# Performance work log

Hardware: AMD Instinct MI355X
Metric: run time of the kernel (lower is better)

## Reference

```python
import jax, jax.numpy as jnp
import numpy as np

E = 32      # particle_embed_dim = q/k/v head out dim
G = 2       # nof_net_types (conv groups)
NEG_SLOPE = 0.01


def _glin(x, w, b, groups):
    """Grouped 1x1 conv on (M, C, 1, 1) == grouped linear.
    x: (M, Cin), w: (Cout, Cin//groups), b: (Cout,)."""
    M = x.shape[0]
    Cout = w.shape[0]
    xg = x.reshape(M, groups, -1)                 # (M, G, Cin/G)
    wg = w.reshape(groups, Cout // groups, -1)    # (G, Cout/G, Cin/G)
    y = jnp.einsum('mgi,goi->mgo', xg, wg).reshape(M, Cout)
    return y + b


def setup_inputs() -> dict:
    key = jax.random.key(0)
    ks = jax.random.split(key, 9)
    B, N = 32, 1024
    s = 0.05
    return {
        'x_e':   jax.random.normal(ks[0], (B, N, G * E), dtype=jnp.float32),
        'w_qkv': jax.random.normal(ks[1], (3 * G * E, E), dtype=jnp.float32) * s,
        'b_qkv': jax.random.normal(ks[2], (3 * G * E,), dtype=jnp.float32) * s,
        'w_h1':  jax.random.normal(ks[3], (G * E, 2 * E), dtype=jnp.float32) * s,
        'b_h1':  jax.random.normal(ks[4], (G * E,), dtype=jnp.float32) * s,
        'w_h10': jax.random.normal(ks[5], (G * E, E), dtype=jnp.float32) * s,
        'b_h10': jax.random.normal(ks[6], (G * E,), dtype=jnp.float32) * s,
        'w_h11': jax.random.normal(ks[7], (G * E, E), dtype=jnp.float32) * s,
        'b_h11': jax.random.normal(ks[8], (G * E,), dtype=jnp.float32) * s,
    }


def reference(x_e, w_qkv, b_qkv, w_h1, b_h1, w_h10, b_h10, w_h11, b_h11):
    B, N, D = x_e.shape                      # D = G*E = 64
    act = lambda z: jnp.where(z >= 0, z, NEG_SLOPE * z)

    # grouped 1x1-conv QKV projection
    qkv = _glin(x_e.reshape(B * N, D), w_qkv, b_qkv, G)        # (B*N, 3*G*E)
    qkv = qkv.reshape(B, N, G, 3, E).transpose(0, 2, 3, 1, 4)  # (B, G, 3, N, E)
    q, k, v = qkv[:, :, 0], qkv[:, :, 1], qkv[:, :, 2]         # each (B, G, N, E)

    # NOTE: module divides k by sqrt(E) and logits by sqrt(E) again -> 1/E total
    scale = 1.0 / E
    ip = jnp.einsum('bgne,bgme->bgnm', q, k) * scale           # (B, G, N, N)
    sip = jax.nn.softmax(ip, axis=-1)
    attn = jnp.einsum('bgnm,bgme->bgne', sip, v)               # (B, G, N, E)

    # concat pre-attention v with attention output, regroup per-particle
    x_xe = jnp.concatenate([v, attn], axis=3)                  # (B, G, N, 2E)
    x_xe = x_xe.transpose(0, 2, 1, 3).reshape(B * N, G * 2 * E)  # (B*N, 128)

    h = act(_glin(x_xe, w_h1, b_h1, G))
    h = act(_glin(h, w_h10, b_h10, G))
    h = act(_glin(h, w_h11, b_h11, G))
    return h.reshape(B * N, G * E, 1, 1)
```

## Files before the change

### kernel.cpp

```cpp
#include <hip/hip_runtime.h>

#define B_ 32
#define N_ 1024
#define NEG 0.01f
#define QSC (1.4426950408889634f/32.0f)

using half8  = __attribute__((ext_vector_type(8))) _Float16;
using half4  = __attribute__((ext_vector_type(4))) _Float16;
using half2  = __attribute__((ext_vector_type(2))) _Float16;
using fp16x2 = __attribute__((ext_vector_type(2))) __fp16;
using floatx4 = __attribute__((ext_vector_type(4))) float;

#if defined(__has_builtin)
#if __has_builtin(__builtin_amdgcn_exp2f)
#define EXP2(x) __builtin_amdgcn_exp2f(x)
#endif
#endif
#ifndef EXP2
#define EXP2(x) exp2f(x)
#endif

__device__ inline half2 pkcvt(float a, float b) {
    fp16x2 r = __builtin_amdgcn_cvt_pkrtz(a, b);
    return __builtin_bit_cast(half2, r);
}

__device__ inline half8 cvt8(float4 a, float4 b) {
    half2 p0 = pkcvt(a.x, a.y);
    half2 p1 = pkcvt(a.z, a.w);
    half2 p2 = pkcvt(b.x, b.y);
    half2 p3 = pkcvt(b.z, b.w);
    half8 h = { p0[0],p0[1], p1[0],p1[1], p2[0],p2[1], p3[0],p3[1] };
    return h;
}

struct __align__(16) Smem {
    _Float16 wsh[96*36];
    float    bsh[96];
    _Float16 Kst[2][128*40];
    _Float16 Vtst[2][32*136];
    union {
        _Float16 qs[128*40];
        _Float16 xs[128*72];
    } u;
    float linv[128];
    float bl1[32], bl10[32], bl11[32];
};

__global__ __launch_bounds__(256, 2) void fused_kernel(
    const float* __restrict__ x, const float* __restrict__ w_qkv, const float* __restrict__ b_qkv,
    const float* __restrict__ w_h1,  const float* __restrict__ b_h1,
    const float* __restrict__ w_h10, const float* __restrict__ b_h10,
    const float* __restrict__ w_h11, const float* __restrict__ b_h11,
    float* __restrict__ out)
{
    __shared__ Smem sm;
    int t = threadIdx.x;
    int bg = blockIdx.x >> 3;
    int qtile = blockIdx.x & 7;
    int b = bg >> 1, g = bg & 1;
    int qbase = qtile * 128;
    int lane = t & 63, w = t >> 6;
    int L15 = lane & 15, quad = lane >> 4;

    for (int idx = t; idx < 96*32; idx += 256) {
        int r = idx >> 5, c = idx & 31;
        float wv = w_qkv[(g*96 + r)*32 + c];
        sm.wsh[r*36 + c] = (_Float16)(r < 32 ? wv*QSC : wv);
    }
    if (t < 96) sm.bsh[t] = b_qkv[g*96 + t];
    if (t < 32) {
        sm.bl1[t]  = b_h1[g*32+t];
        sm.bl10[t] = b_h10[g*32+t];
        sm.bl11[t] = b_h11[g*32+t];
    }
    __syncthreads();

    half8 bwq[2], bwk[2], bwv[2];
    floatx4 cq[2], ck[2], cv[2];
    #pragma unroll
    for (int et = 0; et < 2; et++) {
        bwq[et] = *(const half8*)&sm.wsh[(     et*16 + L15)*36 + quad*8];
        bwk[et] = *(const half8*)&sm.wsh[(32 + et*16 + L15)*36 + quad*8];
        bwv[et] = *(const half8*)&sm.wsh[(64 + et*16 + L15)*36 + quad*8];
        float bq = sm.bsh[     et*16 + L15] * QSC;
        float bk = sm.bsh[32 + et*16 + L15];
        float bv = sm.bsh[64 + et*16 + L15];
        cq[et] = (floatx4){bq,bq,bq,bq};
        ck[et] = (floatx4){bk,bk,bk,bk};
        cv[et] = (floatx4){bv,bv,bv,bv};
    }

    {
        floatx4 dq[2][2];
        #pragma unroll
        for (int mt = 0; mt < 2; mt++) {
            const float* p = x + ((size_t)b*N_ + qbase + w*32 + mt*16 + L15)*64 + g*32 + quad*8;
            half8 axq = cvt8(*(const float4*)p, *(const float4*)(p + 4));
            dq[mt][0] = __builtin_amdgcn_mfma_f32_16x16x32_f16(axq, bwq[0], cq[0], 0,0,0);
            dq[mt][1] = __builtin_amdgcn_mfma_f32_16x16x32_f16(axq, bwq[1], cq[1], 0,0,0);
        }
        #pragma unroll
        for (int mt = 0; mt < 2; mt++)
            #pragma unroll
            for (int et = 0; et < 2; et++)
                #pragma unroll
                for (int r = 0; r < 4; r++)
                    sm.u.qs[(w*32 + mt*16 + quad*4 + r)*40 + et*16 + L15] =
                        (_Float16)dq[mt][et][r];
    }
    __syncthreads();
    half8 bq0 = *(const half8*)&sm.u.qs[(w*32 +      L15)*40 + quad*8];
    half8 bq1 = *(const half8*)&sm.u.qs[(w*32 + 16 + L15)*40 + quad*8];

    float4 xf0[2], xf1[2];
    auto prefetch = [&](int tile) {
        #pragma unroll
        for (int mt = 0; mt < 2; mt++) {
            const float* p = x + ((size_t)b*N_ + tile*128 + w*32 + mt*16 + L15)*64 + g*32 + quad*8;
            xf0[mt] = *(const float4*)p;
            xf1[mt] = *(const float4*)(p + 4);
        }
    };
    auto proj_tile = [&](int tile, int buf) {
        floatx4 dK[2][2], dV[2][2];
        #pragma unroll
        for (int mt = 0; mt < 2; mt++) {
            half8 axk = cvt8(xf0[mt], xf1[mt]);
            dK[mt][0] = __builtin_amdgcn_mfma_f32_16x16x32_f16(axk, bwk[0], ck[0], 0,0,0);
            dK[mt][1] = __builtin_amdgcn_mfma_f32_16x16x32_f16(axk, bwk[1], ck[1], 0,0,0);
            dV[mt][0] = __builtin_amdgcn_mfma_f32_16x16x32_f16(axk, bwv[0], cv[0], 0,0,0);
            dV[mt][1] = __builtin_amdgcn_mfma_f32_16x16x32_f16(axk, bwv[1], cv[1], 0,0,0);
        }
        #pragma unroll
        for (int mt = 0; mt < 2; mt++) {
            int rb = w*32 + mt*16 + quad*4;
            #pragma unroll
            for (int et = 0; et < 2; et++) {
                half2 k01 = pkcvt(dK[mt][et][0], dK[mt][et][1]);
                half2 k23 = pkcvt(dK[mt][et][2], dK[mt][et][3]);
                half2 v01 = pkcvt(dV[mt][et][0], dV[mt][et][1]);
                half2 v23 = pkcvt(dV[mt][et][2], dV[mt][et][3]);
                half4 vh = { v01[0], v01[1], v23[0], v23[1] };
                sm.Kst[buf][(rb+0)*40 + et*16 + L15] = k01[0];
                sm.Kst[buf][(rb+1)*40 + et*16 + L15] = k01[1];
                sm.Kst[buf][(rb+2)*40 + et*16 + L15] = k23[0];
                sm.Kst[buf][(rb+3)*40 + et*16 + L15] = k23[1];
                *(half4*)&sm.Vtst[buf][(et*16 + L15)*136 + rb] = vh;
                if (tile == qtile) {
                    #pragma unroll
                    for (int r = 0; r < 4; r++)
                        sm.u.xs[(rb + r)*72 + et*16 + L15] = vh[r];
                }
            }
        }
    };

    prefetch(0);
    proj_tile(0, 0);
    __syncthreads();

    floatx4 o00 = {0.f,0.f,0.f,0.f}, o01 = o00, o10 = o00, o11 = o00;
    float lsum0 = 0.f, lsum1 = 0.f;

    for (int kt = 0; kt < 8; kt++) {
        int cur = kt & 1;
        if (kt < 7) prefetch(kt + 1);
        #pragma unroll
        for (int mt8 = 0; mt8 < 8; mt8++) {
            half8 ak = *(const half8*)&sm.Kst[cur][(mt8*16 + L15)*40 + quad*8];
            floatx4 zz = {0.f,0.f,0.f,0.f};
            floatx4 s0 = __builtin_amdgcn_mfma_f32_16x16x32_f16(ak, bq0, zz, 0,0,0);
            floatx4 s1 = __builtin_amdgcn_mfma_f32_16x16x32_f16(ak, bq1, zz, 0,0,0);
            float p00 = EXP2(s0.x), p01 = EXP2(s0.y), p02 = EXP2(s0.z), p03 = EXP2(s0.w);
            float p10 = EXP2(s1.x), p11 = EXP2(s1.y), p12 = EXP2(s1.z), p13 = EXP2(s1.w);
            lsum0 += (p00+p01)+(p02+p03);
            lsum1 += (p10+p11)+(p12+p13);
            half2 pa = pkcvt(p00, p01);
            half2 pb = pkcvt(p02, p03);
            half2 pc = pkcvt(p10, p11);
            half2 pd = pkcvt(p12, p13);
            half4 a0 = { pa[0], pa[1], pb[0], pb[1] };
            half4 a1 = { pc[0], pc[1], pd[0], pd[1] };
            half4 bv0 = *(const half4*)&sm.Vtst[cur][      L15*136 + mt8*16 + quad*4];
            half4 bv1 = *(const half4*)&sm.Vtst[cur][(16 + L15)*136 + mt8*16 + quad*4];
            o00 = __builtin_amdgcn_mfma_f32_16x16x16f16(a0, bv0, o00, 0,0,0);
            o01 = __builtin_amdgcn_mfma_f32_16x16x16f16(a0, bv1, o01, 0,0,0);
            o10 = __builtin_amdgcn_mfma_f32_16x16x16f16(a1, bv0, o10, 0,0,0);
            o11 = __builtin_amdgcn_mfma_f32_16x16x16f16(a1, bv1, o11, 0,0,0);
        }
        if (kt < 7) proj_tile(kt + 1, 1 - cur);
        __syncthreads();
    }

    lsum0 += __shfl_xor(lsum0, 16, 64); lsum0 += __shfl_xor(lsum0, 32, 64);
    lsum1 += __shfl_xor(lsum1, 16, 64); lsum1 += __shfl_xor(lsum1, 32, 64);
    if (quad == 0) {
        sm.linv[w*32 +      L15] = 1.0f / lsum0;
        sm.linv[w*32 + 16 + L15] = 1.0f / lsum1;
    }
    __syncthreads();

    {
        const floatx4* ofr[2][2] = { {&o00,&o01}, {&o10,&o11} };
        #pragma unroll
        for (int nt = 0; nt < 2; nt++) {
            float4 li = *(const float4*)&sm.linv[w*32 + nt*16 + quad*4];
            #pragma unroll
            for (int et = 0; et < 2; et++) {
                floatx4 ov = *ofr[nt][et];
                sm.u.xs[(w*32+nt*16+quad*4+0)*72 + 32 + et*16 + L15] = (_Float16)(ov[0]*li.x);
                sm.u.xs[(w*32+nt*16+quad*4+1)*72 + 32 + et*16 + L15] = (_Float16)(ov[1]*li.y);
                sm.u.xs[(w*32+nt*16+quad*4+2)*72 + 32 + et*16 + L15] = (_Float16)(ov[2]*li.z);
                sm.u.xs[(w*32+nt*16+quad*4+3)*72 + 32 + et*16 + L15] = (_Float16)(ov[3]*li.w);
            }
        }
    }
    __syncthreads();

    half4 a1f[2][4], a2f[2][2], a3f[2][2];
    #pragma unroll
    for (int mt = 0; mt < 2; mt++) {
        #pragma unroll
        for (int kt = 0; kt < 4; kt++) {
            float4 f = *(const float4*)(w_h1 + (size_t)(g*32+mt*16+L15)*64 + kt*16 + quad*4);
            half2 ha = pkcvt(f.x, f.y);
            half2 hb = pkcvt(f.z, f.w);
            half4 h = { ha[0], ha[1], hb[0], hb[1] };
            a1f[mt][kt] = h;
        }
        #pragma unroll
        for (int kt = 0; kt < 2; kt++) {
            float4 f = *(const float4*)(w_h10 + (size_t)(g*32+mt*16+L15)*32 + kt*16 + quad*4);
            half2 ha = pkcvt(f.x, f.y);
            half2 hb = pkcvt(f.z, f.w);
            half4 h = { ha[0], ha[1], hb[0], hb[1] };
            a2f[mt][kt] = h;
            float4 f2 = *(const float4*)(w_h11 + (size_t)(g*32+mt*16+L15)*32 + kt*16 + quad*4);
            half2 hc = pkcvt(f2.x, f2.y);
            half2 hd = pkcvt(f2.z, f2.w);
            half4 h2 = { hc[0], hc[1], hd[0], hd[1] };
            a3f[mt][kt] = h2;
        }
    }

    floatx4 d1[2][2];
    #pragma unroll
    for (int mt = 0; mt < 2; mt++) {
        float4 bb = *(const float4*)&sm.bl1[mt*16 + quad*4];
        floatx4 seed = { bb.x, bb.y, bb.z, bb.w };
        d1[mt][0] = seed; d1[mt][1] = seed;
    }
    #pragma unroll
    for (int nt = 0; nt < 2; nt++)
        #pragma unroll
        for (int kt = 0; kt < 4; kt++) {
            half4 b1 = *(const half4*)&sm.u.xs[(w*32+nt*16+L15)*72 + kt*16 + quad*4];
            d1[0][nt] = __builtin_amdgcn_mfma_f32_16x16x16f16(a1f[0][kt], b1, d1[0][nt], 0,0,0);
            d1[1][nt] = __builtin_amdgcn_mfma_f32_16x16x16f16(a1f[1][kt], b1, d1[1][nt], 0,0,0);
        }
    half4 h1b[2][2];
    #pragma unroll
    for (int mt = 0; mt < 2; mt++)
        #pragma unroll
        for (int nt = 0; nt < 2; nt++) {
            float v0 = d1[mt][nt][0]; v0 = (v0>=0.f)?v0:NEG*v0;
            float v1 = d1[mt][nt][1]; v1 = (v1>=0.f)?v1:NEG*v1;
            float v2 = d1[mt][nt][2]; v2 = (v2>=0.f)?v2:NEG*v2;
            float v3 = d1[mt][nt][3]; v3 = (v3>=0.f)?v3:NEG*v3;
            half2 ha = pkcvt(v0, v1);
            half2 hb = pkcvt(v2, v3);
            half4 h = { ha[0], ha[1], hb[0], hb[1] };
            h1b[mt][nt] = h;
        }
    floatx4 d2[2][2];
    #pragma unroll
    for (int mt = 0; mt < 2; mt++) {
        float4 bb = *(const float4*)&sm.bl10[mt*16 + quad*4];
        floatx4 seed = { bb.x, bb.y, bb.z, bb.w };
        d2[mt][0] = seed; d2[mt][1] = seed;
    }
    #pragma unroll
    for (int mt = 0; mt < 2; mt++)
        #pragma unroll
        for (int nt = 0; nt < 2; nt++)
            #pragma unroll
            for (int kt = 0; kt < 2; kt++)
                d2[mt][nt] = __builtin_amdgcn_mfma_f32_16x16x16f16(a2f[mt][kt], h1b[kt][nt], d2[mt][nt], 0,0,0);
    half4 h2b[2][2];
    #pragma unroll
    for (int mt = 0; mt < 2; mt++)
        #pragma unroll
        for (int nt = 0; nt < 2; nt++) {
            float v0 = d2[mt][nt][0]; v0 = (v0>=0.f)?v0:NEG*v0;
            float v1 = d2[mt][nt][1]; v1 = (v1>=0.f)?v1:NEG*v1;
            float v2 = d2[mt][nt][2]; v2 = (v2>=0.f)?v2:NEG*v2;
            float v3 = d2[mt][nt][3]; v3 = (v3>=0.f)?v3:NEG*v3;
            half2 ha = pkcvt(v0, v1);
            half2 hb = pkcvt(v2, v3);
            half4 h = { ha[0], ha[1], hb[0], hb[1] };
            h2b[mt][nt] = h;
        }
    floatx4 d3[2][2];
    #pragma unroll
    for (int mt = 0; mt < 2; mt++) {
        float4 bb = *(const float4*)&sm.bl11[mt*16 + quad*4];
        floatx4 seed = { bb.x, bb.y, bb.z, bb.w };
        d3[mt][0] = seed; d3[mt][1] = seed;
    }
    #pragma unroll
    for (int mt = 0; mt < 2; mt++)
        #pragma unroll
        for (int nt = 0; nt < 2; nt++)
            #pragma unroll
            for (int kt = 0; kt < 2; kt++)
                d3[mt][nt] = __builtin_amdgcn_mfma_f32_16x16x16f16(a3f[mt][kt], h2b[kt][nt], d3[mt][nt], 0,0,0);
    #pragma unroll
    for (int mt = 0; mt < 2; mt++)
        #pragma unroll
        for (int nt = 0; nt < 2; nt++) {
            float4 ov;
            ov.x = d3[mt][nt][0]; ov.x = (ov.x>=0.f)?ov.x:NEG*ov.x;
            ov.y = d3[mt][nt][1]; ov.y = (ov.y>=0.f)?ov.y:NEG*ov.y;
            ov.z = d3[mt][nt][2]; ov.z = (ov.z>=0.f)?ov.z:NEG*ov.z;
            ov.w = d3[mt][nt][3]; ov.w = (ov.w>=0.f)?ov.w:NEG*ov.w;
            *(float4*)(out + ((size_t)b*N_ + qbase + w*32 + nt*16 + L15)*64 + g*32 + mt*16 + quad*4) = ov;
        }
}

extern "C" void kernel_launch(void* const* d_in, const int* in_sizes, int n_in,
                              void* d_out, int out_size, void* d_ws, size_t ws_size,
                              hipStream_t stream) {
    const float* x_e   = (const float*)d_in[0];
    const float* w_qkv = (const float*)d_in[1];
    const float* b_qkv = (const float*)d_in[2];
    const float* w_h1  = (const float*)d_in[3];
    const float* b_h1  = (const float*)d_in[4];
    const float* w_h10 = (const float*)d_in[5];
    const float* b_h10 = (const float*)d_in[6];
    const float* w_h11 = (const float*)d_in[7];
    const float* b_h11 = (const float*)d_in[8];
    float* out = (float*)d_out;

    hipLaunchKernelGGL(fused_kernel, dim3(B_*2*8), dim3(256), 0, stream,
                       x_e, w_qkv, b_qkv, w_h1, b_h1, w_h10, b_h10, w_h11, b_h11, out);
}
```

Measured before the change: 98.57 us.

## Halve query tile to 64 rows and raise occupancy with overlapped LDS

Each block now handles 64 query rows instead of 128, and streams keys in 64-row tiles over 16 iterations. The grid doubles to 1024 blocks and launch bounds allow 4 blocks per CU. Shared memory is shrunk by overlaying the weight staging, Q staging, K/V double buffers and the MLP input buffer in unions. The block's own V rows are recomputed from x after the loop instead of copied during projection. The aim is more resident waves to hide latency, at the cost of duplicating the K/V projection across twice as many blocks, twice as many barriers, and fewer MFMAs per LDS load.

```diff
diff --git a/kernel.cpp b/kernel.cpp
--- a/kernel.cpp
+++ b/kernel.cpp
@@ -35,19 +35,22 @@
 }
 
 struct __align__(16) Smem {
-    _Float16 wsh[96*36];
-    float    bsh[96];
-    _Float16 Kst[2][128*40];
-    _Float16 Vtst[2][32*136];
     union {
-        _Float16 qs[128*40];
-        _Float16 xs[128*72];
+        struct {
+            _Float16 Kst[2][64*40];
+            _Float16 Vtst[2][32*72];
+            union {
+                struct { _Float16 wsh[96*36]; float bsh[96]; } wg;
+                _Float16 qs[64*40];
+            } pq;
+        } lp;
+        _Float16 xs[64*72];
     } u;
-    float linv[128];
+    float linv[64];
     float bl1[32], bl10[32], bl11[32];
 };
 
-__global__ __launch_bounds__(256, 2) void fused_kernel(
+__global__ __launch_bounds__(256, 4) void fused_kernel(
     const float* __restrict__ x, const float* __restrict__ w_qkv, const float* __restrict__ b_qkv,
     const float* __restrict__ w_h1,  const float* __restrict__ b_h1,
     const float* __restrict__ w_h10, const float* __restrict__ b_h10,
@@ -56,19 +59,19 @@
 {
     __shared__ Smem sm;
     int t = threadIdx.x;
-    int bg = blockIdx.x >> 3;
-    int qtile = blockIdx.x & 7;
+    int bg = blockIdx.x >> 4;
+    int qtile = blockIdx.x & 15;
     int b = bg >> 1, g = bg & 1;
-    int qbase = qtile * 128;
+    int qbase = qtile * 64;
     int lane = t & 63, w = t >> 6;
     int L15 = lane & 15, quad = lane >> 4;
 
     for (int idx = t; idx < 96*32; idx += 256) {
         int r = idx >> 5, c = idx & 31;
         float wv = w_qkv[(g*96 + r)*32 + c];
-        sm.wsh[r*36 + c] = (_Float16)(r < 32 ? wv*QSC : wv);
-    }
-    if (t < 96) sm.bsh[t] = b_qkv[g*96 + t];
+        sm.u.lp.pq.wg.wsh[r*36 + c] = (_Float16)(r < 32 ? wv*QSC : wv);
+    }
+    if (t < 96) sm.u.lp.pq.wg.bsh[t] = b_qkv[g*96 + t];
     if (t < 32) {
         sm.bl1[t]  = b_h1[g*32+t];
         sm.bl10[t] = b_h10[g*32+t];
@@ -80,143 +83,116 @@
     floatx4 cq[2], ck[2], cv[2];
     #pragma unroll
     for (int et = 0; et < 2; et++) {
-        bwq[et] = *(const half8*)&sm.wsh[(     et*16 + L15)*36 + quad*8];
-        bwk[et] = *(const half8*)&sm.wsh[(32 + et*16 + L15)*36 + quad*8];
-        bwv[et] = *(const half8*)&sm.wsh[(64 + et*16 + L15)*36 + quad*8];
-        float bq = sm.bsh[     et*16 + L15] * QSC;
-        float bk = sm.bsh[32 + et*16 + L15];
-        float bv = sm.bsh[64 + et*16 + L15];
+        bwq[et] = *(const half8*)&sm.u.lp.pq.wg.wsh[(     et*16 + L15)*36 + quad*8];
+        bwk[et] = *(const half8*)&sm.u.lp.pq.wg.wsh[(32 + et*16 + L15)*36 + quad*8];
+        bwv[et] = *(const half8*)&sm.u.lp.pq.wg.wsh[(64 + et*16 + L15)*36 + quad*8];
+        float bq = sm.u.lp.pq.wg.bsh[     et*16 + L15] * QSC;
+        float bk = sm.u.lp.pq.wg.bsh[32 + et*16 + L15];
+        float bv = sm.u.lp.pq.wg.bsh[64 + et*16 + L15];
         cq[et] = (floatx4){bq,bq,bq,bq};
         ck[et] = (floatx4){bk,bk,bk,bk};
         cv[et] = (floatx4){bv,bv,bv,bv};
     }
+    __syncthreads();
 
     {
-        floatx4 dq[2][2];
-        #pragma unroll
-        for (int mt = 0; mt < 2; mt++) {
-            const float* p = x + ((size_t)b*N_ + qbase + w*32 + mt*16 + L15)*64 + g*32 + quad*8;
-            half8 axq = cvt8(*(const float4*)p, *(const float4*)(p + 4));
-            dq[mt][0] = __builtin_amdgcn_mfma_f32_16x16x32_f16(axq, bwq[0], cq[0], 0,0,0);
-            dq[mt][1] = __builtin_amdgcn_mfma_f32_16x16x32_f16(axq, bwq[1], cq[1], 0,0,0);
-        }
-        #pragma unroll
-        for (int mt = 0; mt < 2; mt++)
-            #pragma unroll
-            for (int et = 0; et < 2; et++)
-                #pragma unroll
-                for (int r = 0; r < 4; r++)
-                    sm.u.qs[(w*32 + mt*16 + quad*4 + r)*40 + et*16 + L15] =
-                        (_Float16)dq[mt][et][r];
-    }
+        const float* p = x + ((size_t)b*N_ + qbase + w*16 + L15)*64 + g*32 + quad*8;
+        half8 axq = cvt8(*(const float4*)p, *(const float4*)(p + 4));
+        floatx4 dq0 = __builtin_amdgcn_mfma_f32_16x16x32_f16(axq, bwq[0], cq[0], 0,0,0);
+        floatx4 dq1 = __builtin_amdgcn_mfma_f32_16x16x32_f16(axq, bwq[1], cq[1], 0,0,0);
+        #pragma unroll
+        for (int r = 0; r < 4; r++) {
+            sm.u.lp.pq.qs[(w*16 + quad*4 + r)*40 +      L15] = (_Float16)dq0[r];
+            sm.u.lp.pq.qs[(w*16 + quad*4 + r)*40 + 16 + L15] = (_Float16)dq1[r];
+        }
+    }
+    half8 bq = *(const half8*)&sm.u.lp.pq.qs[(w*16 + L15)*40 + quad*8];
+
+    float4 xf0, xf1;
+    auto prefetch = [&](int tile) {
+        const float* p = x + ((size_t)b*N_ + tile*64 + w*16 + L15)*64 + g*32 + quad*8;
+        xf0 = *(const float4*)p;
+        xf1 = *(const float4*)(p + 4);
+    };
+    auto proj_tile = [&](int buf) {
+        half8 axk = cvt8(xf0, xf1);
+        floatx4 dK[2], dV[2];
+        #pragma unroll
+        for (int et = 0; et < 2; et++) {
+            dK[et] = __builtin_amdgcn_mfma_f32_16x16x32_f16(axk, bwk[et], ck[et], 0,0,0);
+            dV[et] = __builtin_amdgcn_mfma_f32_16x16x32_f16(axk, bwv[et], cv[et], 0,0,0);
+        }
+        int rb = w*16 + quad*4;
+        #pragma unroll
+        for (int et = 0; et < 2; et++) {
+            half2 k01 = pkcvt(dK[et][0], dK[et][1]);
+            half2 k23 = pkcvt(dK[et][2], dK[et][3]);
+            half2 v01 = pkcvt(dV[et][0], dV[et][1]);
+            half2 v23 = pkcvt(dV[et][2], dV[et][3]);
+            half4 vh = { v01[0], v01[1], v23[0], v23[1] };
+            sm.u.lp.Kst[buf][(rb+0)*40 + et*16 + L15] = k01[0];
+            sm.u.lp.Kst[buf][(rb+1)*40 + et*16 + L15] = k01[1];
+            sm.u.lp.Kst[buf][(rb+2)*40 + et*16 + L15] = k23[0];
+            sm.u.lp.Kst[buf][(rb+3)*40 + et*16 + L15] = k23[1];
+            *(half4*)&sm.u.lp.Vtst[buf][(et*16 + L15)*72 + rb] = vh;
+        }
+    };
+
+    prefetch(0);
+    proj_tile(0);
     __syncthreads();
-    half8 bq0 = *(const half8*)&sm.u.qs[(w*32 +      L15)*40 + quad*8];
-    half8 bq1 = *(const half8*)&sm.u.qs[(w*32 + 16 + L15)*40 + quad*8];
-
-    float4 xf0[2], xf1[2];
-    auto prefetch = [&](int tile) {
-        #pragma unroll
-        for (int mt = 0; mt < 2; mt++) {
-            const float* p = x + ((size_t)b*N_ + tile*128 + w*32 + mt*16 + L15)*64 + g*32 + quad*8;
-            xf0[mt] = *(const float4*)p;
-            xf1[mt] = *(const float4*)(p + 4);
-        }
-    };
-    auto proj_tile = [&](int tile, int buf) {
-        floatx4 dK[2][2], dV[2][2];
-        #pragma unroll
-        for (int mt = 0; mt < 2; mt++) {
-            half8 axk = cvt8(xf0[mt], xf1[mt]);
-            dK[mt][0] = __builtin_amdgcn_mfma_f32_16x16x32_f16(axk, bwk[0], ck[0], 0,0,0);
-            dK[mt][1] = __builtin_amdgcn_mfma_f32_16x16x32_f16(axk, bwk[1], ck[1], 0,0,0);
-            dV[mt][0] = __builtin_amdgcn_mfma_f32_16x16x32_f16(axk, bwv[0], cv[0], 0,0,0);
-            dV[mt][1] = __builtin_amdgcn_mfma_f32_16x16x32_f16(axk, bwv[1], cv[1], 0,0,0);
-        }
-        #pragma unroll
-        for (int mt = 0; mt < 2; mt++) {
-            int rb = w*32 + mt*16 + quad*4;
-            #pragma unroll
-            for (int et = 0; et < 2; et++) {
-                half2 k01 = pkcvt(dK[mt][et][0], dK[mt][et][1]);
-                half2 k23 = pkcvt(dK[mt][et][2], dK[mt][et][3]);
-                half2 v01 = pkcvt(dV[mt][et][0], dV[mt][et][1]);
-                half2 v23 = pkcvt(dV[mt][et][2], dV[mt][et][3]);
-                half4 vh = { v01[0], v01[1], v23[0], v23[1] };
-                sm.Kst[buf][(rb+0)*40 + et*16 + L15] = k01[0];
-                sm.Kst[buf][(rb+1)*40 + et*16 + L15] = k01[1];
-                sm.Kst[buf][(rb+2)*40 + et*16 + L15] = k23[0];
-                sm.Kst[buf][(rb+3)*40 + et*16 + L15] = k23[1];
-                *(half4*)&sm.Vtst[buf][(et*16 + L15)*136 + rb] = vh;
-                if (tile == qtile) {
-                    #pragma unroll
-                    for (int r = 0; r < 4; r++)
-                        sm.u.xs[(rb + r)*72 + et*16 + L15] = vh[r];
-                }
-            }
-        }
-    };
-
-    prefetch(0);
-    proj_tile(0, 0);
-    __syncthreads();
-
-    floatx4 o00 = {0.f,0.f,0.f,0.f}, o01 = o00, o10 = o00, o11 = o00;
-    float lsum0 = 0.f, lsum1 = 0.f;
-
-    for (int kt = 0; kt < 8; kt++) {
+
+    floatx4 o0 = {0.f,0.f,0.f,0.f}, o1 = o0;
+    float lsum = 0.f;
+
+    for (int kt = 0; kt < 16; kt++) {
         int cur = kt & 1;
-        if (kt < 7) prefetch(kt + 1);
-        #pragma unroll
-        for (int mt8 = 0; mt8 < 8; mt8++) {
-            half8 ak = *(const half8*)&sm.Kst[cur][(mt8*16 + L15)*40 + quad*8];
+        if (kt < 15) prefetch(kt + 1);
+        #pragma unroll
+        for (int mt8 = 0; mt8 < 4; mt8++) {
+            half8 ak = *(const half8*)&sm.u.lp.Kst[cur][(mt8*16 + L15)*40 + quad*8];
             floatx4 zz = {0.f,0.f,0.f,0.f};
-            floatx4 s0 = __builtin_amdgcn_mfma_f32_16x16x32_f16(ak, bq0, zz, 0,0,0);
-            floatx4 s1 = __builtin_amdgcn_mfma_f32_16x16x32_f16(ak, bq1, zz, 0,0,0);
-            float p00 = EXP2(s0.x), p01 = EXP2(s0.y), p02 = EXP2(s0.z), p03 = EXP2(s0.w);
-            float p10 = EXP2(s1.x), p11 = EXP2(s1.y), p12 = EXP2(s1.z), p13 = EXP2(s1.w);
-            lsum0 += (p00+p01)+(p02+p03);
-            lsum1 += (p10+p11)+(p12+p13);
-            half2 pa = pkcvt(p00, p01);
-            half2 pb = pkcvt(p02, p03);
-            half2 pc = pkcvt(p10, p11);
-            half2 pd = pkcvt(p12, p13);
+            floatx4 s = __builtin_amdgcn_mfma_f32_16x16x32_f16(ak, bq, zz, 0,0,0);
+            float p0 = EXP2(s.x), p1 = EXP2(s.y), p2 = EXP2(s.z), p3 = EXP2(s.w);
+            lsum += (p0+p1)+(p2+p3);
+            half2 pa = pkcvt(p0, p1);
+            half2 pb = pkcvt(p2, p3);
             half4 a0 = { pa[0], pa[1], pb[0], pb[1] };
-            half4 a1 = { pc[0], pc[1], pd[0], pd[1] };
-            half4 bv0 = *(const half4*)&sm.Vtst[cur][      L15*136 + mt8*16 + quad*4];
-            half4 bv1 = *(const half4*)&sm.Vtst[cur][(16 + L15)*136 + mt8*16 + quad*4];
-            o00 = __builtin_amdgcn_mfma_f32_16x16x16f16(a0, bv0, o00, 0,0,0);
-            o01 = __builtin_amdgcn_mfma_f32_16x16x16f16(a0, bv1, o01, 0,0,0);
-            o10 = __builtin_amdgcn_mfma_f32_16x16x16f16(a1, bv0, o10, 0,0,0);
-            o11 = __builtin_amdgcn_mfma_f32_16x16x16f16(a1, bv1, o11, 0,0,0);
-        }
-        if (kt < 7) proj_tile(kt + 1, 1 - cur);
+            half4 bv0 = *(const half4*)&sm.u.lp.Vtst[cur][      L15*72 + mt8*16 + quad*4];
+            half4 bv1 = *(const half4*)&sm.u.lp.Vtst[cur][(16 + L15)*72 + mt8*16 + quad*4];
+            o0 = __builtin_amdgcn_mfma_f32_16x16x16f16(a0, bv0, o0, 0,0,0);
+            o1 = __builtin_amdgcn_mfma_f32_16x16x16f16(a0, bv1, o1, 0,0,0);
+        }
+        if (kt < 15) proj_tile(1 - cur);
         __syncthreads();
     }
 
-    lsum0 += __shfl_xor(lsum0, 16, 64); lsum0 += __shfl_xor(lsum0, 32, 64);
-    lsum1 += __shfl_xor(lsum1, 16, 64); lsum1 += __shfl_xor(lsum1, 32, 64);
-    if (quad == 0) {
-        sm.linv[w*32 +      L15] = 1.0f / lsum0;
-        sm.linv[w*32 + 16 + L15] = 1.0f / lsum1;
-    }
-    __syncthreads();
+    lsum += __shfl_xor(lsum, 16, 64); lsum += __shfl_xor(lsum, 32, 64);
+    if (quad == 0) sm.linv[w*16 + L15] = 1.0f / lsum;
 
     {
-        const floatx4* ofr[2][2] = { {&o00,&o01}, {&o10,&o11} };
-        #pragma unroll
-        for (int nt = 0; nt < 2; nt++) {
-            float4 li = *(const float4*)&sm.linv[w*32 + nt*16 + quad*4];
-            #pragma unroll
-            for (int et = 0; et < 2; et++) {
-                floatx4 ov = *ofr[nt][et];
-                sm.u.xs[(w*32+nt*16+quad*4+0)*72 + 32 + et*16 + L15] = (_Float16)(ov[0]*li.x);
-                sm.u.xs[(w*32+nt*16+quad*4+1)*72 + 32 + et*16 + L15] = (_Float16)(ov[1]*li.y);
-                sm.u.xs[(w*32+nt*16+quad*4+2)*72 + 32 + et*16 + L15] = (_Float16)(ov[2]*li.z);
-                sm.u.xs[(w*32+nt*16+quad*4+3)*72 + 32 + et*16 + L15] = (_Float16)(ov[3]*li.w);
-            }
-        }
-    }
-    __syncthreads();
+        const float* p = x + ((size_t)b*N_ + qbase + w*16 + L15)*64 + g*32 + quad*8;
+        half8 axv = cvt8(*(const float4*)p, *(const float4*)(p + 4));
+        floatx4 dv0 = __builtin_amdgcn_mfma_f32_16x16x32_f16(axv, bwv[0], cv[0], 0,0,0);
+        floatx4 dv1 = __builtin_amdgcn_mfma_f32_16x16x32_f16(axv, bwv[1], cv[1], 0,0,0);
+        #pragma unroll
+        for (int r = 0; r < 4; r++) {
+            sm.u.xs[(w*16 + quad*4 + r)*72 +      L15] = (_Float16)dv0[r];
+            sm.u.xs[(w*16 + quad*4 + r)*72 + 16 + L15] = (_Float16)dv1[r];
+        }
+    }
+    {
+        float4 li = *(const float4*)&sm.linv[w*16 + quad*4];
+        const floatx4* ofr[2] = { &o0, &o1 };
+        #pragma unroll
+        for (int et = 0; et < 2; et++) {
+            floatx4 ov = *ofr[et];
+            sm.u.xs[(w*16+quad*4+0)*72 + 32 + et*16 + L15] = (_Float16)(ov[0]*li.x);
+            sm.u.xs[(w*16+quad*4+1)*72 + 32 + et*16 + L15] = (_Float16)(ov[1]*li.y);
+            sm.u.xs[(w*16+quad*4+2)*72 + 32 + et*16 + L15] = (_Float16)(ov[2]*li.z);
+            sm.u.xs[(w*16+quad*4+3)*72 + 32 + et*16 + L15] = (_Float16)(ov[3]*li.w);
+        }
+    }
 
     half4 a1f[2][4], a2f[2][2], a3f[2][2];
     #pragma unroll
@@ -244,88 +220,73 @@
         }
     }
 
-    floatx4 d1[2][2];
+    floatx4 d1[2];
     #pragma unroll
     for (int mt = 0; mt < 2; mt++) {
         float4 bb = *(const float4*)&sm.bl1[mt*16 + quad*4];
-        floatx4 seed = { bb.x, bb.y, bb.z, bb.w };
-        d1[mt][0] = seed; d1[mt][1] = seed;
-    }
-    #pragma unroll
-    for (int nt = 0; nt < 2; nt++)
-        #pragma unroll
-        for (int kt = 0; kt < 4; kt++) {
-            half4 b1 = *(const half4*)&sm.u.xs[(w*32+nt*16+L15)*72 + kt*16 + quad*4];
-            d1[0][nt] = __builtin_amdgcn_mfma_f32_16x16x16f16(a1f[0][kt], b1, d1[0][nt], 0,0,0);
-            d1[1][nt] = __builtin_amdgcn_mfma_f32_16x16x16f16(a1f[1][kt], b1, d1[1][nt], 0,0,0);
-        }
-    half4 h1b[2][2];
+        d1[mt] = (floatx4){ bb.x, bb.y, bb.z, bb.w };
+    }
+    #pragma unroll
+    for (int kt = 0; kt < 4; kt++) {
+        half4 b1 = *(const half4*)&sm.u.xs[(w*16+L15)*72 + kt*16 + quad*4];
+        d1[0] = __builtin_amdgcn_mfma_f32_16x16x16f16(a1f[0][kt], b1, d1[0], 0,0,0);
+        d1[1] = __builtin_amdgcn_mfma_f32_16x16x16f16(a1f[1][kt], b1, d1[1], 0,0,0);
+    }
+    half4 h1b[2];
+    #pragma unroll
+    for (int mt = 0; mt < 2; mt++) {
+        float v0 = d1[mt][0]; v0 = (v0>=0.f)?v0:NEG*v0;
+        float v1 = d1[mt][1]; v1 = (v1>=0.f)?v1:NEG*v1;
+        float v2 = d1[mt][2]; v2 = (v2>=0.f)?v2:NEG*v2;
+        float v3 = d1[mt][3]; v3 = (v3>=0.f)?v3:NEG*v3;
+        half2 ha = pkcvt(v0, v1);
+        half2 hb = pkcvt(v2, v3);
+        half4 h = { ha[0], ha[1], hb[0], hb[1] };
+        h1b[mt] = h;
+    }
+    floatx4 d2[2];
+    #pragma unroll
+    for (int mt = 0; mt < 2; mt++) {
+        float4 bb = *(const float4*)&sm.bl10[mt*16 + quad*4];
+        d2[mt] = (floatx4){ bb.x, bb.y, bb.z, bb.w };
+    }
     #pragma unroll
     for (int mt = 0; mt < 2; mt++)
         #pragma unroll
-        for (int nt = 0; nt < 2; nt++) {
-            float v0 = d1[mt][nt][0]; v0 = (v0>=0.f)?v0:NEG*v0;
-            float v1 = d1[mt][nt][1]; v1 = (v1>=0.f)?v1:NEG*v1;
-            float v2 = d1[mt][nt][2]; v2 = (v2>=0.f)?v2:NEG*v2;
-            float v3 = d1[mt][nt][3]; v3 = (v3>=0.f)?v3:NEG*v3;
-            half2 ha = pkcvt(v0, v1);
-            half2 hb = pkcvt(v2, v3);
-            half4 h = { ha[0], ha[1], hb[0], hb[1] };
-            h1b[mt][nt] = h;
-        }
-    floatx4 d2[2][2];
-    #pragma unroll
-    for (int mt = 0; mt < 2; mt++) {
-        float4 bb = *(const float4*)&sm.bl10[mt*16 + quad*4];
-        floatx4 seed = { bb.x, bb.y, bb.z, bb.w };
-        d2[mt][0] = seed; d2[mt][1] = seed;
+        for (int kt = 0; kt < 2; kt++)
+            d2[mt] = __builtin_amdgcn_mfma_f32_16x16x16f16(a2f[mt][kt], h1b[kt], d2[mt], 0,0,0);
+    half4 h2b[2];
+    #pragma unroll
+    for (int mt = 0; mt < 2; mt++) {
+        float v0 = d2[mt][0]; v0 = (v0>=0.f)?v0:NEG*v0;
+        float v1 = d2[mt][1]; v1 = (v1>=0.f)?v1:NEG*v1;
+        float v2 = d2[mt][2]; v2 = (v2>=0.f)?v2:NEG*v2;
+        float v3 = d2[mt][3]; v3 = (v3>=0.f)?v3:NEG*v3;
+        half2 ha = pkcvt(v0, v1);
+        half2 hb = pkcvt(v2, v3);
+        half4 h = { ha[0], ha[1], hb[0], hb[1] };
+        h2b[mt] = h;
+    }
+    floatx4 d3[2];
+    #pragma unroll
+    for (int mt = 0; mt < 2; mt++) {
+        float4 bb = *(const float4*)&sm.bl11[mt*16 + quad*4];
+        d3[mt] = (floatx4){ bb.x, bb.y, bb.z, bb.w };
     }
     #pragma unroll
     for (int mt = 0; mt < 2; mt++)
         #pragma unroll
-        for (int nt = 0; nt < 2; nt++)
-            #pragma unroll
-            for (int kt = 0; kt < 2; kt++)
-                d2[mt][nt] = __builtin_amdgcn_mfma_f32_16x16x16f16(a2f[mt][kt], h1b[kt][nt], d2[mt][nt], 0,0,0);
-    half4 h2b[2][2];
-    #pragma unroll
-    for (int mt = 0; mt < 2; mt++)
-        #pragma unroll
-        for (int nt = 0; nt < 2; nt++) {
-            float v0 = d2[mt][nt][0]; v0 = (v0>=0.f)?v0:NEG*v0;
-            float v1 = d2[mt][nt][1]; v1 = (v1>=0.f)?v1:NEG*v1;
-            float v2 = d2[mt][nt][2]; v2 = (v2>=0.f)?v2:NEG*v2;
-            float v3 = d2[mt][nt][3]; v3 = (v3>=0.f)?v3:NEG*v3;
-            half2 ha = pkcvt(v0, v1);
-            half2 hb = pkcvt(v2, v3);
-            half4 h = { ha[0], ha[1], hb[0], hb[1] };
-            h2b[mt][nt] = h;
-        }
-    floatx4 d3[2][2];
-    #pragma unroll
-    for (int mt = 0; mt < 2; mt++) {
-        float4 bb = *(const float4*)&sm.bl11[mt*16 + quad*4];
-        floatx4 seed = { bb.x, bb.y, bb.z, bb.w };
-        d3[mt][0] = seed; d3[mt][1] = seed;
-    }
-    #pragma unroll
-    for (int mt = 0; mt < 2; mt++)
-        #pragma unroll
-        for (int nt = 0; nt < 2; nt++)
-            #pragma unroll
-            for (int kt = 0; kt < 2; kt++)
-                d3[mt][nt] = __builtin_amdgcn_mfma_f32_16x16x16f16(a3f[mt][kt], h2b[kt][nt], d3[mt][nt], 0,0,0);
-    #pragma unroll
-    for (int mt = 0; mt < 2; mt++)
-        #pragma unroll
-        for (int nt = 0; nt < 2; nt++) {
-            float4 ov;
-            ov.x = d3[mt][nt][0]; ov.x = (ov.x>=0.f)?ov.x:NEG*ov.x;
-            ov.y = d3[mt][nt][1]; ov.y = (ov.y>=0.f)?ov.y:NEG*ov.y;
-            ov.z = d3[mt][nt][2]; ov.z = (ov.z>=0.f)?ov.z:NEG*ov.z;
-            ov.w = d3[mt][nt][3]; ov.w = (ov.w>=0.f)?ov.w:NEG*ov.w;
-            *(float4*)(out + ((size_t)b*N_ + qbase + w*32 + nt*16 + L15)*64 + g*32 + mt*16 + quad*4) = ov;
-        }
+        for (int kt = 0; kt < 2; kt++)
+            d3[mt] = __builtin_amdgcn_mfma_f32_16x16x16f16(a3f[mt][kt], h2b[kt], d3[mt], 0,0,0);
+    #pragma unroll
+    for (int mt = 0; mt < 2; mt++) {
+        float4 ov;
+        ov.x = d3[mt][0]; ov.x = (ov.x>=0.f)?ov.x:NEG*ov.x;
+        ov.y = d3[mt][1]; ov.y = (ov.y>=0.f)?ov.y:NEG*ov.y;
+        ov.z = d3[mt][2]; ov.z = (ov.z>=0.f)?ov.z:NEG*ov.z;
+        ov.w = d3[mt][3]; ov.w = (ov.w>=0.f)?ov.w:NEG*ov.w;
+        *(float4*)(out + ((size_t)b*N_ + qbase + w*16 + L15)*64 + g*32 + mt*16 + quad*4) = ov;
+    }
 }
 
 extern "C" void kernel_launch(void* const* d_in, const int* in_sizes, int n_in,
@@ -342,6 +303,6 @@
     const float* b_h11 = (const float*)d_in[8];
     float* out = (float*)d_out;
 
-    hipLaunchKernelGGL(fused_kernel, dim3(B_*2*8), dim3(256), 0, stream,
+    hipLaunchKernelGGL(fused_kernel, dim3(B_*2*16), dim3(256), 0, stream,
                        x_e, w_qkv, b_qkv, w_h1, b_h1, w_h10, b_h10, w_h11, b_h11, out);
 }
```

Result: slower. 107.9 us (+9.5%).

## Deepen x prefetch, drop wave-local barriers, shrink LDS, and reorder block mapping

Applied to the files above, without the earlier changes.

The global loads of x are now double-buffered in registers and issued two tiles ahead, so load latency overlaps with more attention work. Several __syncthreads are removed where each wave only reads LDS rows it wrote itself. The QKV weight staging now shares a union with the Q/X buffers, and the V transpose stride is reduced from 136 to 132, which cuts LDS use and changes the bank mapping. The block index is remapped so all (batch, group) pairs for one query tile run together. The pre-attention V for the block's own tile is recomputed from x at the end instead of being stored conditionally inside the projection loop. In exchange, register pressure rises and there is a small amount of redundant MFMA work and global reads.

```diff
diff --git a/kernel.cpp b/kernel.cpp
--- a/kernel.cpp
+++ b/kernel.cpp
@@ -35,11 +35,10 @@
 }
 
 struct __align__(16) Smem {
-    _Float16 wsh[96*36];
-    float    bsh[96];
     _Float16 Kst[2][128*40];
-    _Float16 Vtst[2][32*136];
+    _Float16 Vtst[2][32*132];
     union {
+        struct { _Float16 wsh[96*36]; float bsh[96]; } wg;
         _Float16 qs[128*40];
         _Float16 xs[128*72];
     } u;
@@ -56,8 +55,8 @@
 {
     __shared__ Smem sm;
     int t = threadIdx.x;
-    int bg = blockIdx.x >> 3;
-    int qtile = blockIdx.x & 7;
+    int bg = blockIdx.x & 63;
+    int qtile = blockIdx.x >> 6;
     int b = bg >> 1, g = bg & 1;
     int qbase = qtile * 128;
     int lane = t & 63, w = t >> 6;
@@ -66,9 +65,9 @@
     for (int idx = t; idx < 96*32; idx += 256) {
         int r = idx >> 5, c = idx & 31;
         float wv = w_qkv[(g*96 + r)*32 + c];
-        sm.wsh[r*36 + c] = (_Float16)(r < 32 ? wv*QSC : wv);
-    }
-    if (t < 96) sm.bsh[t] = b_qkv[g*96 + t];
+        sm.u.wg.wsh[r*36 + c] = (_Float16)(r < 32 ? wv*QSC : wv);
+    }
+    if (t < 96) sm.u.wg.bsh[t] = b_qkv[g*96 + t];
     if (t < 32) {
         sm.bl1[t]  = b_h1[g*32+t];
         sm.bl10[t] = b_h10[g*32+t];
@@ -80,84 +79,75 @@
     floatx4 cq[2], ck[2], cv[2];
     #pragma unroll
     for (int et = 0; et < 2; et++) {
-        bwq[et] = *(const half8*)&sm.wsh[(     et*16 + L15)*36 + quad*8];
-        bwk[et] = *(const half8*)&sm.wsh[(32 + et*16 + L15)*36 + quad*8];
-        bwv[et] = *(const half8*)&sm.wsh[(64 + et*16 + L15)*36 + quad*8];
-        float bq = sm.bsh[     et*16 + L15] * QSC;
-        float bk = sm.bsh[32 + et*16 + L15];
-        float bv = sm.bsh[64 + et*16 + L15];
+        bwq[et] = *(const half8*)&sm.u.wg.wsh[(     et*16 + L15)*36 + quad*8];
+        bwk[et] = *(const half8*)&sm.u.wg.wsh[(32 + et*16 + L15)*36 + quad*8];
+        bwv[et] = *(const half8*)&sm.u.wg.wsh[(64 + et*16 + L15)*36 + quad*8];
+        float bq = sm.u.wg.bsh[     et*16 + L15] * QSC;
+        float bk = sm.u.wg.bsh[32 + et*16 + L15];
+        float bv = sm.u.wg.bsh[64 + et*16 + L15];
         cq[et] = (floatx4){bq,bq,bq,bq};
         ck[et] = (floatx4){bk,bk,bk,bk};
         cv[et] = (floatx4){bv,bv,bv,bv};
     }
+    __syncthreads();
 
     {
-        floatx4 dq[2][2];
         #pragma unroll
         for (int mt = 0; mt < 2; mt++) {
             const float* p = x + ((size_t)b*N_ + qbase + w*32 + mt*16 + L15)*64 + g*32 + quad*8;
             half8 axq = cvt8(*(const float4*)p, *(const float4*)(p + 4));
-            dq[mt][0] = __builtin_amdgcn_mfma_f32_16x16x32_f16(axq, bwq[0], cq[0], 0,0,0);
-            dq[mt][1] = __builtin_amdgcn_mfma_f32_16x16x32_f16(axq, bwq[1], cq[1], 0,0,0);
-        }
-        #pragma unroll
-        for (int mt = 0; mt < 2; mt++)
-            #pragma unroll
-            for (int et = 0; et < 2; et++)
-                #pragma unroll
-                for (int r = 0; r < 4; r++)
-                    sm.u.qs[(w*32 + mt*16 + quad*4 + r)*40 + et*16 + L15] =
-                        (_Float16)dq[mt][et][r];
-    }
-    __syncthreads();
+            floatx4 dq0 = __builtin_amdgcn_mfma_f32_16x16x32_f16(axq, bwq[0], cq[0], 0,0,0);
+            floatx4 dq1 = __builtin_amdgcn_mfma_f32_16x16x32_f16(axq, bwq[1], cq[1], 0,0,0);
+            #pragma unroll
+            for (int r = 0; r < 4; r++) {
+                sm.u.qs[(w*32 + mt*16 + quad*4 + r)*40 +      L15] = (_Float16)dq0[r];
+                sm.u.qs[(w*32 + mt*16 + quad*4 + r)*40 + 16 + L15] = (_Float16)dq1[r];
+            }
+        }
+    }
     half8 bq0 = *(const half8*)&sm.u.qs[(w*32 +      L15)*40 + quad*8];
     half8 bq1 = *(const half8*)&sm.u.qs[(w*32 + 16 + L15)*40 + quad*8];
 
-    float4 xf0[2], xf1[2];
-    auto prefetch = [&](int tile) {
+    float4 xf0[2][2], xf1[2][2];
+    auto prefetch = [&](int tile, int pp) {
         #pragma unroll
         for (int mt = 0; mt < 2; mt++) {
             const float* p = x + ((size_t)b*N_ + tile*128 + w*32 + mt*16 + L15)*64 + g*32 + quad*8;
-            xf0[mt] = *(const float4*)p;
-            xf1[mt] = *(const float4*)(p + 4);
+            xf0[pp][mt] = *(const float4*)p;
+            xf1[pp][mt] = *(const float4*)(p + 4);
         }
     };
-    auto proj_tile = [&](int tile, int buf) {
-        floatx4 dK[2][2], dV[2][2];
+    auto proj_tile = [&](int buf, int pp) {
         #pragma unroll
         for (int mt = 0; mt < 2; mt++) {
-            half8 axk = cvt8(xf0[mt], xf1[mt]);
-            dK[mt][0] = __builtin_amdgcn_mfma_f32_16x16x32_f16(axk, bwk[0], ck[0], 0,0,0);
-            dK[mt][1] = __builtin_amdgcn_mfma_f32_16x16x32_f16(axk, bwk[1], ck[1], 0,0,0);
-            dV[mt][0] = __builtin_amdgcn_mfma_f32_16x16x32_f16(axk, bwv[0], cv[0], 0,0,0);
-            dV[mt][1] = __builtin_amdgcn_mfma_f32_16x16x32_f16(axk, bwv[1], cv[1], 0,0,0);
-        }
-        #pragma unroll
-        for (int mt = 0; mt < 2; mt++) {
+            half8 axk = cvt8(xf0[pp][mt], xf1[pp][mt]);
+            floatx4 dK[2], dV[2];
+            #pragma unroll
+            for (int et = 0; et < 2; et++) {
+                dK[et] = __builtin_amdgcn_mfma_f32_16x16x32_f16(axk, bwk[et], ck[et], 0,0,0);
+                dV[et] = __builtin_amdgcn_mfma_f32_16x16x32_f16(axk, bwv[et], cv[et], 0,0,0);
+            }
             int rb = w*32 + mt*16 + quad*4;
             #pragma unroll
             for (int et = 0; et < 2; et++) {
-                half2 k01 = pkcvt(dK[mt][et][0], dK[mt][et][1]);
-                half2 k23 = pkcvt(dK[mt][et][2], dK[mt][et][3]);
-                half2 v01 = pkcvt(dV[mt][et][0], dV[mt][et][1]);
-                half2 v23 = pkcvt(dV[mt][et][2], dV[mt][et][3]);
+                half2 k01 = pkcvt(dK[et][0], dK[et][1]);
+                half2 k23 = pkcvt(dK[et][2], dK[et][3]);
+                half2 v01 = pkcvt(dV[et][0], dV[et][1]);
+                half2 v23 = pkcvt(dV[et][2], dV[et][3]);
                 half4 vh = { v01[0], v01[1], v23[0], v23[1] };
                 sm.Kst[buf][(rb+0)*40 + et*16 + L15] = k01[0];
                 sm.Kst[buf][(rb+1)*40 + et*16 + L15] = k01[1];
                 sm.Kst[buf][(rb+2)*40 + et*16 + L15] = k23[0];
                 sm.Kst[buf][(rb+3)*40 + et*16 + L15] = k23[1];
-                *(half4*)&sm.Vtst[buf][(et*16 + L15)*136 + rb] = vh;
-                if (tile == qtile) {
-                    #pragma unroll
-                    for (int r = 0; r < 4; r++)
-                        sm.u.xs[(rb + r)*72 + et*16 + L15] = vh[r];
-                }
+                *(half4*)&sm.Vtst[buf][(et*16 + L15)*132 + rb] = vh;
             }
         }
     };
 
-    prefetch(0);
+    prefetch(0, 0);
     proj_tile(0, 0);
+    prefetch(1, 1);
+    prefetch(2, 0);
     __syncthreads();
 
     floatx4 o00 = {0.f,0.f,0.f,0.f}, o01 = o00, o10 = o00, o11 = o00;
@@ -165,10 +155,9 @@
 
     for (int kt = 0; kt < 8; kt++) {
         int cur = kt & 1;
-        if (kt < 7) prefetch(kt + 1);
-        #pragma unroll
-        for (int mt8 = 0; mt8 < 8; mt8++) {
-            half8 ak = *(const half8*)&sm.Kst[cur][(mt8*16 + L15)*40 + quad*8];
+        #pragma unroll
+        for (int m8 = 0; m8 < 8; m8++) {
+            half8 ak = *(const half8*)&sm.Kst[cur][(m8*16 + L15)*40 + quad*8];
             floatx4 zz = {0.f,0.f,0.f,0.f};
             floatx4 s0 = __builtin_amdgcn_mfma_f32_16x16x32_f16(ak, bq0, zz, 0,0,0);
             floatx4 s1 = __builtin_amdgcn_mfma_f32_16x16x32_f16(ak, bq1, zz, 0,0,0);
@@ -182,14 +171,15 @@
             half2 pd = pkcvt(p12, p13);
             half4 a0 = { pa[0], pa[1], pb[0], pb[1] };
             half4 a1 = { pc[0], pc[1], pd[0], pd[1] };
-            half4 bv0 = *(const half4*)&sm.Vtst[cur][      L15*136 + mt8*16 + quad*4];
-            half4 bv1 = *(const half4*)&sm.Vtst[cur][(16 + L15)*136 + mt8*16 + quad*4];
+            half4 bv0 = *(const half4*)&sm.Vtst[cur][      L15*132 + m8*16 + quad*4];
+            half4 bv1 = *(const half4*)&sm.Vtst[cur][(16 + L15)*132 + m8*16 + quad*4];
             o00 = __builtin_amdgcn_mfma_f32_16x16x16f16(a0, bv0, o00, 0,0,0);
             o01 = __builtin_amdgcn_mfma_f32_16x16x16f16(a0, bv1, o01, 0,0,0);
             o10 = __builtin_amdgcn_mfma_f32_16x16x16f16(a1, bv0, o10, 0,0,0);
             o11 = __builtin_amdgcn_mfma_f32_16x16x16f16(a1, bv1, o11, 0,0,0);
         }
-        if (kt < 7) proj_tile(kt + 1, 1 - cur);
+        if (kt < 7) proj_tile(1 - cur, (kt + 1) & 1);
+        if (kt < 5) prefetch(kt + 3, (kt + 1) & 1);
         __syncthreads();
     }
 
@@ -199,8 +189,19 @@
         sm.linv[w*32 +      L15] = 1.0f / lsum0;
         sm.linv[w*32 + 16 + L15] = 1.0f / lsum1;
     }
-    __syncthreads();
-
+
+    #pragma unroll
+    for (int mt = 0; mt < 2; mt++) {
+        const float* p = x + ((size_t)b*N_ + qbase + w*32 + mt*16 + L15)*64 + g*32 + quad*8;
+        half8 axv = cvt8(*(const float4*)p, *(const float4*)(p + 4));
+        floatx4 dv0 = __builtin_amdgcn_mfma_f32_16x16x32_f16(axv, bwv[0], cv[0], 0,0,0);
+        floatx4 dv1 = __builtin_amdgcn_mfma_f32_16x16x32_f16(axv, bwv[1], cv[1], 0,0,0);
+        #pragma unroll
+        for (int r = 0; r < 4; r++) {
+            sm.u.xs[(w*32 + mt*16 + quad*4 + r)*72 +      L15] = (_Float16)dv0[r];
+            sm.u.xs[(w*32 + mt*16 + quad*4 + r)*72 + 16 + L15] = (_Float16)dv1[r];
+        }
+    }
     {
         const floatx4* ofr[2][2] = { {&o00,&o01}, {&o10,&o11} };
         #pragma unroll
@@ -216,7 +217,6 @@
             }
         }
     }
-    __syncthreads();
 
     half4 a1f[2][4], a2f[2][2], a3f[2][2];
     #pragma unroll
```

New measurement: 99.20 us. About the same (+0.6%).
